# Kernel optimization log

Hardware: AMD Instinct MI355X
Metric: run time of the kernel (lower is better)

## Reference

```python
import jax, jax.numpy as jnp
import numpy as np

HID = 3584; NH = 16; NKV = 8; HD = 256; S = 3072; WIN = 2048
SOFTCAP = 50.0; QSCALE = 256.0 ** -0.5  # query_pre_attn_scalar = 256
NEG = -2.3819763e38


def _rope(x, cos, sin):
    # x: (B, S, heads, HD); cos/sin: (S, HD//2). Gemma half-split complex RoPE.
    x1, x2 = jnp.split(x, 2, axis=-1)
    c = cos[None, :, None, :]
    s = sin[None, :, None, :]
    return jnp.concatenate([x1 * c - x2 * s, x1 * s + x2 * c], axis=-1)


def setup_inputs() -> dict:
    key = jax.random.key(0)
    k1, k2, k3 = jax.random.split(key, 3)
    hidden_states = jax.random.normal(k1, (1, S, HID), jnp.float32)
    qkv_w = jax.random.normal(k2, (NH * HD + 2 * NKV * HD, HID), jnp.float32) * 0.02
    o_w = jax.random.normal(k3, (HID, NH * HD), jnp.float32) * 0.02
    inv = 1.0 / (10000.0 ** (jnp.arange(0, HD, 2, dtype=jnp.float32) / HD))
    ang = jnp.arange(S, dtype=jnp.float32)[:, None] * inv[None, :]
    freqs_cis = jnp.stack([jnp.cos(ang), jnp.sin(ang)], axis=-1)  # (S, HD//2, 2)
    kv_write_indices = jnp.arange(S, dtype=jnp.int32)
    k_cache = jnp.zeros((1, S, NKV, HD), jnp.float32)
    v_cache = jnp.zeros((1, S, NKV, HD), jnp.float32)
    i = jnp.arange(S)[:, None]
    j = jnp.arange(S)[None, :]
    mask = jnp.where(j <= i, 0.0, NEG).astype(jnp.float32)[None, None]  # causal (1,1,S,S)
    return dict(hidden_states=hidden_states, freqs_cis=freqs_cis,
                kv_write_indices=kv_write_indices, k_cache=k_cache, v_cache=v_cache,
                mask=mask, qkv_w=qkv_w, o_w=o_w)


def reference(hidden_states, freqs_cis, kv_write_indices, k_cache, v_cache, mask, qkv_w, o_w):
    B, L, _ = hidden_states.shape
    qkv = hidden_states @ qkv_w.T  # (B, L, 8192)
    xq, xk, xv = jnp.split(qkv, [NH * HD, NH * HD + NKV * HD], axis=-1)
    xq = xq.reshape(B, L, NH, HD)
    xk = xk.reshape(B, L, NKV, HD)
    xv = xv.reshape(B, L, NKV, HD)
    cos, sin = freqs_cis[..., 0], freqs_cis[..., 1]
    xq = _rope(xq, cos, sin)
    xk = _rope(xk, cos, sin)
    # KV cache index_copy_ on dim 1
    k_all = k_cache.at[:, kv_write_indices].set(xk)  # (B, T, NKV, HD)
    v_all = v_cache.at[:, kv_write_indices].set(xv)
    T = k_all.shape[1]
    G = NH // NKV  # queries per kv head; grouped einsum avoids repeat_interleave
    q = (xq * QSCALE).transpose(0, 2, 1, 3).reshape(B, NKV, G, L, HD)
    k = k_all.transpose(0, 2, 1, 3)  # (B, NKV, T, HD)
    v = v_all.transpose(0, 2, 1, 3)
    scores = jnp.einsum('bkgsd,bktd->bkgst', q, k)
    # logit softcapping
    scores = jnp.tanh(scores / SOFTCAP) * SOFTCAP
    # sliding-window band applied on top of the provided (causal) mask
    i = jnp.arange(L)[:, None]
    j = jnp.arange(T)[None, :]
    band = (j >= i - WIN + 1) & (j <= i + WIN - 1)
    m = jnp.where(band, mask, NEG)  # (1,1,L,T)
    scores = scores + m[:, :, None]  # broadcast over group dim
    probs = jax.nn.softmax(scores.astype(jnp.float32), axis=-1).astype(q.dtype)
    out = jnp.einsum('bkgst,bktd->bkgsd', probs, v)
    out = out.reshape(B, NH, L, HD).transpose(0, 2, 1, 3).reshape(B, L, NH * HD)
    return out @ o_w.T
```

## Files before the change

kernel.cpp:

```cpp
#include <hip/hip_runtime.h>

#define S_LEN 3072
#define NHQ 16
#define NKVH 8
#define HDIM 256
#define WIN 2048
#define QKV_COLS 8192

typedef __bf16 bf16x8 __attribute__((ext_vector_type(8)));
typedef float f32x4 __attribute__((ext_vector_type(4)));

__device__ __forceinline__ unsigned short f2bf(float f) {
    union { float f; unsigned u; } v; v.f = f;
    unsigned r = v.u + 0x7FFFu + ((v.u >> 16) & 1u);
    return (unsigned short)(r >> 16);
}
__device__ __forceinline__ float bf2f(unsigned short u) {
    union { unsigned u; float f; } v; v.u = ((unsigned)u) << 16; return v.f;
}

typedef __attribute__((address_space(3))) void lds_void_t;
typedef const __attribute__((address_space(1))) void glb_void_t;
__device__ __forceinline__ void async16(const void* g, void* l) {
    __builtin_amdgcn_global_load_lds((glb_void_t*)g, (lds_void_t*)l, 16, 0, 0);
}

__global__ __launch_bounds__(256) void cast_bf16_kernel(const float* __restrict__ src,
                                                        unsigned short* __restrict__ dst,
                                                        int n) {
    int i = (blockIdx.x * 256 + threadIdx.x) * 4;
    if (i >= n) return;
    float4 v = *(const float4*)(src + i);
    ushort4 o;
    o.x = f2bf(v.x); o.y = f2bf(v.y); o.z = f2bf(v.z); o.w = f2bf(v.w);
    *(ushort4*)(dst + i) = o;
}

template <int OUT_BF16>
__global__ __launch_bounds__(256) void gemm_bt(const unsigned short* __restrict__ A,
                                               const unsigned short* __restrict__ B,
                                               void* __restrict__ Cv,
                                               int N, int K) {
    __shared__ __align__(16) unsigned short At[128 * 32];
    __shared__ __align__(16) unsigned short Bt[128 * 32];
    const int tid = threadIdx.x;
    const int wid = tid >> 6, lane = tid & 63;
    const int ln = lane & 15, quad = lane >> 4;
    const int bm = blockIdx.y, bn = blockIdx.x;
    const int wm = wid >> 1, wn = wid & 1;

    const f32x4 fzero = {0.f, 0.f, 0.f, 0.f};
    f32x4 acc[4][4];
#pragma unroll
    for (int i = 0; i < 4; i++) {
#pragma unroll
        for (int j = 0; j < 4; j++) acc[i][j] = fzero;
    }

    const unsigned short* gA = A + (size_t)(bm * 128 + wid * 32 + (lane >> 2)) * K + (lane & 3) * 8;
    const unsigned short* gB = B + (size_t)(bn * 128 + wid * 32 + (lane >> 2)) * K + (lane & 3) * 8;
    unsigned short* lA = At + wid * 32 * 32;
    unsigned short* lB = Bt + wid * 32 * 32;

    for (int k0 = 0; k0 < K; k0 += 32) {
        async16(gA + k0, lA);
        async16(gA + k0 + 16 * K, lA + 16 * 32);
        async16(gB + k0, lB);
        async16(gB + k0 + 16 * K, lB + 16 * 32);
        __syncthreads();

        bf16x8 af[4], bfr[4];
#pragma unroll
        for (int mt = 0; mt < 4; mt++)
            af[mt] = *(const bf16x8*)(At + (wm * 64 + mt * 16 + ln) * 32 + quad * 8);
#pragma unroll
        for (int nt = 0; nt < 4; nt++)
            bfr[nt] = *(const bf16x8*)(Bt + (wn * 64 + nt * 16 + ln) * 32 + quad * 8);
#pragma unroll
        for (int mt = 0; mt < 4; mt++) {
#pragma unroll
            for (int nt = 0; nt < 4; nt++)
                acc[mt][nt] = __builtin_amdgcn_mfma_f32_16x16x32_bf16(af[mt], bfr[nt], acc[mt][nt], 0, 0, 0);
        }
        __syncthreads();
    }

    const int row0 = bm * 128 + wm * 64 + quad * 4;
    const int col0 = bn * 128 + wn * 64 + ln;
    if (OUT_BF16) {
        unsigned short* C = (unsigned short*)Cv;
#pragma unroll
        for (int mt = 0; mt < 4; mt++) {
#pragma unroll
            for (int nt = 0; nt < 4; nt++) {
#pragma unroll
                for (int rr = 0; rr < 4; rr++)
                    C[(size_t)(row0 + mt * 16 + rr) * N + col0 + nt * 16] = f2bf(acc[mt][nt][rr]);
            }
        }
    } else {
        float* C = (float*)Cv;
#pragma unroll
        for (int mt = 0; mt < 4; mt++) {
#pragma unroll
            for (int nt = 0; nt < 4; nt++) {
#pragma unroll
                for (int rr = 0; rr < 4; rr++)
                    C[(size_t)(row0 + mt * 16 + rr) * N + col0 + nt * 16] = acc[mt][nt][rr];
            }
        }
    }
}

__global__ __launch_bounds__(256) void rope_kernel(const unsigned short* __restrict__ qkv,
                                                   const float* __restrict__ freqs,
                                                   const int* __restrict__ kvidx,
                                                   unsigned short* __restrict__ Qb,
                                                   unsigned short* __restrict__ Kb) {
    int t = blockIdx.x * 256 + threadIdx.x;
    int d = t & 127;
    int t2 = t >> 7;
    int hh = t2 % 24;
    int pos = t2 / 24;
    if (pos >= S_LEN) return;
    float2 cs = *(const float2*)(freqs + ((size_t)pos * 128 + d) * 2);
    if (hh < NHQ) {
        const unsigned short* src = qkv + (size_t)pos * QKV_COLS + hh * HDIM + d;
        float x1 = bf2f(src[0]), x2 = bf2f(src[128]);
        float o1 = (x1 * cs.x - x2 * cs.y) * 0.0625f;
        float o2 = (x1 * cs.y + x2 * cs.x) * 0.0625f;
        unsigned short* dst = Qb + ((size_t)hh * S_LEN + pos) * HDIM + d;
        dst[0] = f2bf(o1);
        dst[128] = f2bf(o2);
    } else {
        int kvh = hh - NHQ;
        const unsigned short* src = qkv + (size_t)pos * QKV_COLS + NHQ * HDIM + kvh * HDIM + d;
        float x1 = bf2f(src[0]), x2 = bf2f(src[128]);
        float o1 = x1 * cs.x - x2 * cs.y;
        float o2 = x1 * cs.y + x2 * cs.x;
        int wpos = kvidx[pos];
        unsigned short* dst = Kb + ((size_t)kvh * S_LEN + wpos) * HDIM + d;
        dst[0] = f2bf(o1);
        dst[128] = f2bf(o2);
    }
}

__global__ __launch_bounds__(256) void vtrans_kernel(const unsigned short* __restrict__ qkv,
                                                     const int* __restrict__ kvidx,
                                                     unsigned short* __restrict__ Vbt) {
    __shared__ unsigned short T[64][72];
    int pos0 = blockIdx.x * 64;
    int c0 = blockIdx.y * 64;
    int a = threadIdx.x >> 6;
    int b = threadIdx.x & 63;
#pragma unroll
    for (int r = 0; r < 16; r++) {
        int pl = r * 4 + a;
        T[pl][b] = qkv[(size_t)(pos0 + pl) * QKV_COLS + 6144 + c0 + b];
    }
    __syncthreads();
    int wpos = kvidx[pos0 + b];
#pragma unroll
    for (int r = 0; r < 16; r++) {
        int cl = r * 4 + a;
        Vbt[(size_t)(c0 + cl) * S_LEN + wpos] = T[b][cl];
    }
}

__global__ __launch_bounds__(512, 4) void attn_kernel(const unsigned short* __restrict__ Qb,
                                                      const unsigned short* __restrict__ Kb,
                                                      const unsigned short* __restrict__ Vbt,
                                                      float* __restrict__ Acc,
                                                      float* __restrict__ Ps,
                                                      unsigned short* __restrict__ attn_out) {
    __shared__ __align__(16) unsigned short Kl[2][32 * 256];
    __shared__ __align__(16) unsigned short Vl[2][256 * 32];
    __shared__ __align__(16) unsigned short Plb[8][16][40];

    const int kv = blockIdx.x / 96;
    const int it = 95 - (blockIdx.x % 96);
    int qb, sub, nc;
    if (it < 16)      { qb = it; sub = 0; nc = 1; }
    else if (it < 48) { int e = it - 16; qb = 16 + (e >> 1); sub = e & 1; nc = 2; }
    else              { int e = it - 48; qb = 32 + e / 3; sub = e % 3; nc = 3; }

    const int q0 = qb * 64;
    const int tid = threadIdx.x;
    const int wid = tid >> 6, lane = tid & 63;
    const int ln = lane & 15, quad = lane >> 4;
    const int h = kv * 2 + (wid >> 2);
    const int wrow = (wid & 3) * 16;

    bf16x8 qf[8];
    {
        const unsigned short* qrow = Qb + ((size_t)h * S_LEN + q0 + wrow + ln) * HDIM;
#pragma unroll
        for (int k0 = 0; k0 < 8; k0++)
            qf[k0] = *(const bf16x8*)(qrow + k0 * 32 + quad * 8);
    }

    const f32x4 fzero = {0.f, 0.f, 0.f, 0.f};
    f32x4 acc[16];
#pragma unroll
    for (int t = 0; t < 16; t++) acc[t] = fzero;
    float ps[4] = {0.f, 0.f, 0.f, 0.f};

    const int imin = q0 + wrow;
    const int imax = imin + 15;
    const int irow = imin + quad * 4;

    const int t_lo = (q0 >= WIN) ? ((q0 - (WIN - 1)) >> 5) : 0;
    const int t_hi = (q0 + 63) >> 5;
    const int tn = t_hi - t_lo + 1;
    const int ts = t_lo + (tn * sub) / nc;
    const int te = t_lo + (tn * (sub + 1)) / nc;

    const unsigned short* kSrcA = Kb + ((size_t)kv * S_LEN + (tid >> 5)) * HDIM
                                  + ((tid & 31) ^ ((tid >> 5) & 7)) * 8;
    const unsigned short* vSrcA = Vbt + ((size_t)kv * HDIM + (tid >> 2)) * S_LEN
                                  + ((tid & 3) ^ ((tid >> 3) & 3)) * 8;

    {
        const int p0s = ts * 32;
        const unsigned short* ks = kSrcA + (size_t)p0s * HDIM;
        const unsigned short* vs = vSrcA + p0s;
        async16(ks,                 &Kl[0][tid * 8]);
        async16(ks + 16 * HDIM,     &Kl[0][(512 + tid) * 8]);
        async16(vs,                 &Vl[0][tid * 8]);
        async16(vs + 128 * S_LEN,   &Vl[0][(512 + tid) * 8]);
    }

    const int kswz = (ln & 7);
    const unsigned short* vbb_off = (const unsigned short*)0; (void)vbb_off;
    int cur = 0;

    for (int tt = ts; tt < te; tt++) {
        asm volatile("s_waitcnt vmcnt(0)" ::: "memory");
        __builtin_amdgcn_s_barrier();
        asm volatile("" ::: "memory");

        if (tt + 1 < te) {
            const int p0n = (tt + 1) * 32;
            const unsigned short* ks = kSrcA + (size_t)p0n * HDIM;
            const unsigned short* vs = vSrcA + p0n;
            async16(ks,                 &Kl[cur ^ 1][tid * 8]);
            async16(ks + 16 * HDIM,     &Kl[cur ^ 1][(512 + tid) * 8]);
            async16(vs,                 &Vl[cur ^ 1][tid * 8]);
            async16(vs + 128 * S_LEN,   &Vl[cur ^ 1][(512 + tid) * 8]);
        }

        const int p0 = tt * 32;
        const bool live = (p0 <= imax) && (p0 + 31 >= imin - WIN + 1);
        if (live) {
            const unsigned short* kb = Kl[cur];
            f32x4 s0 = fzero, s1 = fzero;
#pragma unroll
            for (int k0 = 0; k0 < 8; k0++) {
                const int cp = (((k0 * 4 + quad) ^ kswz) << 3);
                bf16x8 b0 = *(const bf16x8*)(kb + ln * HDIM + cp);
                s0 = __builtin_amdgcn_mfma_f32_16x16x32_bf16(qf[k0], b0, s0, 0, 0, 0);
            }
#pragma unroll
            for (int k0 = 0; k0 < 8; k0++) {
                const int cp = (((k0 * 4 + quad) ^ kswz) << 3);
                bf16x8 b1 = *(const bf16x8*)(kb + (16 + ln) * HDIM + cp);
                s1 = __builtin_amdgcn_mfma_f32_16x16x32_bf16(qf[k0], b1, s1, 0, 0, 0);
            }

            const bool full = (p0 + 31 <= imin) && (p0 >= imax - WIN + 1);
#pragma unroll
            for (int r = 0; r < 4; r++) {
                float z0 = __expf(s0[r] * 0.04f);
                float z1 = __expf(s1[r] * 0.04f);
                float t0 = fmaf(-100.f, __builtin_amdgcn_rcpf(z0 + 1.f), 50.f);
                float t1 = fmaf(-100.f, __builtin_amdgcn_rcpf(z1 + 1.f), 50.f);
                float p0v = __expf(t0);
                float p1v = __expf(t1);
                if (!full) {
                    const int i = irow + r;
                    int j0 = p0 + ln, j1 = p0 + 16 + ln;
                    p0v = ((j0 <= i) && (j0 + WIN > i)) ? p0v : 0.f;
                    p1v = ((j1 <= i) && (j1 + WIN > i)) ? p1v : 0.f;
                }
                ps[r] += p0v + p1v;
                Plb[wid][quad * 4 + r][ln] = f2bf(p0v);
                Plb[wid][quad * 4 + r][16 + ln] = f2bf(p1v);
            }
            bf16x8 pa = *(const bf16x8*)(&Plb[wid][ln][quad * 8]);
            const unsigned short* vbb = Vl[cur] + ln * 32 + ((quad ^ ((ln >> 1) & 3)) << 3);
#pragma unroll
            for (int t = 0; t < 16; t++) {
                bf16x8 vb = *(const bf16x8*)(vbb + t * 512);
                acc[t] = __builtin_amdgcn_mfma_f32_16x16x32_bf16(pa, vb, acc[t], 0, 0, 0);
            }
        }
        cur ^= 1;
    }

    float psr[4];
#pragma unroll
    for (int r = 0; r < 4; r++) {
        float s = ps[r];
#pragma unroll
        for (int o = 1; o <= 8; o <<= 1)
            s += __shfl_xor(s, o);
        psr[r] = s;
    }

    if (nc == 1) {
#pragma unroll
        for (int t = 0; t < 16; t++) {
#pragma unroll
            for (int r = 0; r < 4; r++) {
                float o = acc[t][r] * __builtin_amdgcn_rcpf(psr[r]);
                attn_out[(size_t)(irow + r) * 4096 + h * HDIM + t * 16 + ln] = f2bf(o);
            }
        }
    } else {
        if (ln == 0) {
#pragma unroll
            for (int r = 0; r < 4; r++)
                atomicAdd(&Ps[h * S_LEN + irow + r], psr[r]);
        }
#pragma unroll
        for (int t = 0; t < 16; t++) {
#pragma unroll
            for (int r = 0; r < 4; r++)
                atomicAdd(&Acc[((size_t)h * S_LEN + irow + r) * HDIM + t * 16 + ln], acc[t][r]);
        }
    }
}

__global__ __launch_bounds__(256) void norm_kernel(const float* __restrict__ Acc,
                                                   const float* __restrict__ Ps,
                                                   unsigned short* __restrict__ attn_out) {
    int row = blockIdx.x * 4 + (threadIdx.x >> 6);
    int lane = threadIdx.x & 63;
    int h = row >> 11;
    int pos = 1024 + (row & 2047);
    float4 a = *(const float4*)(Acc + ((size_t)h * S_LEN + pos) * HDIM + lane * 4);
    float inv = __builtin_amdgcn_rcpf(Ps[h * S_LEN + pos]);
    ushort4 o;
    o.x = f2bf(a.x * inv); o.y = f2bf(a.y * inv);
    o.z = f2bf(a.z * inv); o.w = f2bf(a.w * inv);
    *(ushort4*)(attn_out + (size_t)pos * 4096 + h * HDIM + lane * 4) = o;
}

extern "C" void kernel_launch(void* const* d_in, const int* in_sizes, int n_in,
                              void* d_out, int out_size, void* d_ws, size_t ws_size,
                              hipStream_t stream) {
    (void)in_sizes; (void)n_in; (void)out_size; (void)ws_size;
    const float* hidden = (const float*)d_in[0];
    const float* freqs  = (const float*)d_in[1];
    const int* kvidx    = (const int*)d_in[2];
    const float* qkv_w  = (const float*)d_in[6];
    const float* o_w    = (const float*)d_in[7];
    float* out = (float*)d_out;

    char* ws = (char*)d_ws;
    unsigned short* hs_bf   = (unsigned short*)(ws);
    unsigned short* w1_bf   = (unsigned short*)(ws + 22020096);
    unsigned short* w2_bf   = (unsigned short*)(ws + 80740352);
    unsigned short* qkv_bf  = (unsigned short*)(ws + 110100480);
    unsigned short* Qb      = (unsigned short*)(ws + 160432128);
    unsigned short* Kb      = (unsigned short*)(ws + 185597952);
    unsigned short* Vbt     = (unsigned short*)(ws + 198180864);
    unsigned short* attn_bf = (unsigned short*)(ws + 210763776);

    float* Acc = (float*)(ws + 110100480);
    float* Ps  = (float*)(ws);

    cast_bf16_kernel<<<10752, 256, 0, stream>>>(hidden, hs_bf, 11010048);
    cast_bf16_kernel<<<28672, 256, 0, stream>>>(qkv_w, w1_bf, 29360128);
    cast_bf16_kernel<<<14336, 256, 0, stream>>>(o_w, w2_bf, 14680064);

    gemm_bt<1><<<dim3(64, 24), 256, 0, stream>>>(hs_bf, w1_bf, (void*)qkv_bf, 8192, 3584);

    rope_kernel<<<36864, 256, 0, stream>>>(qkv_bf, freqs, kvidx, Qb, Kb);
    vtrans_kernel<<<dim3(48, 32), 256, 0, stream>>>(qkv_bf, kvidx, Vbt);

    hipMemsetAsync(Acc, 0, (size_t)16 * 3072 * 256 * 4, stream);
    hipMemsetAsync(Ps, 0, (size_t)16 * 3072 * 4, stream);

    attn_kernel<<<768, 512, 0, stream>>>(Qb, Kb, Vbt, Acc, Ps, attn_bf);
    norm_kernel<<<8192, 256, 0, stream>>>(Acc, Ps, attn_bf);

    gemm_bt<0><<<dim3(28, 24), 256, 0, stream>>>(attn_bf, w2_bf, (void*)out, 3584, 4096);
}
```

Baseline: 943.2 us.

## Rework attention to 32x32 MFMA tiles with per-head 128-row blocks and split-K rebalancing

The attention kernel now uses 32x32x16 bf16 MFMA instead of 16x16x32. Each 256-thread block handles one query head and 128 query rows, with each wave owning 32 rows. The KV range is split into up to five chunks to balance work, and the normalization kernel is adjusted to the new split boundaries. The GEMM also remaps workgroup ids across 8 groups, aiming for better L2 or XCD locality. Each block now loads its own KV tiles, which doubles KV traffic relative to the previous sharing across two query heads. More chunks also mean more atomic accumulation, and the larger accumulators raise register pressure.

```diff
diff --git a/kernel.cpp b/kernel.cpp
--- a/kernel.cpp
+++ b/kernel.cpp
@@ -9,6 +9,7 @@
 
 typedef __bf16 bf16x8 __attribute__((ext_vector_type(8)));
 typedef float f32x4 __attribute__((ext_vector_type(4)));
+typedef float f32x16 __attribute__((ext_vector_type(16)));
 
 __device__ __forceinline__ unsigned short f2bf(float f) {
     union { float f; unsigned u; } v; v.f = f;
@@ -46,7 +47,19 @@
     const int tid = threadIdx.x;
     const int wid = tid >> 6, lane = tid & 63;
     const int ln = lane & 15, quad = lane >> 4;
-    const int bm = blockIdx.y, bn = blockIdx.x;
+
+    int bm, bn;
+    {
+        const int nwg = gridDim.x * gridDim.y;
+        int orig = blockIdx.y * gridDim.x + blockIdx.x;
+        int wg = orig;
+        if ((nwg & 7) == 0) {
+            const int cpx = nwg >> 3;
+            wg = (orig & 7) * cpx + (orig >> 3);
+        }
+        bm = wg / gridDim.x;
+        bn = wg % gridDim.x;
+    }
     const int wm = wid >> 1, wn = wid & 1;
 
     const f32x4 fzero = {0.f, 0.f, 0.f, 0.f};
@@ -167,7 +180,7 @@
     }
 }
 
-__global__ __launch_bounds__(512, 4) void attn_kernel(const unsigned short* __restrict__ Qb,
+__global__ __launch_bounds__(256, 1) void attn_kernel(const unsigned short* __restrict__ Qb,
                                                       const unsigned short* __restrict__ Kb,
                                                       const unsigned short* __restrict__ Vbt,
                                                       float* __restrict__ Acc,
@@ -175,42 +188,47 @@
                                                       unsigned short* __restrict__ attn_out) {
     __shared__ __align__(16) unsigned short Kl[2][32 * 256];
     __shared__ __align__(16) unsigned short Vl[2][256 * 32];
-    __shared__ __align__(16) unsigned short Plb[8][16][40];
-
-    const int kv = blockIdx.x / 96;
-    const int it = 95 - (blockIdx.x % 96);
+    __shared__ __align__(16) unsigned short Plb[4][1024];
+
+    const int h = blockIdx.x / 80;
+    const int it = 79 - (blockIdx.x % 80);
     int qb, sub, nc;
-    if (it < 16)      { qb = it; sub = 0; nc = 1; }
-    else if (it < 48) { int e = it - 16; qb = 16 + (e >> 1); sub = e & 1; nc = 2; }
-    else              { int e = it - 48; qb = 32 + e / 3; sub = e % 3; nc = 3; }
-
-    const int q0 = qb * 64;
+    if (it < 4)       { qb = it; sub = 0; nc = 1; }
+    else if (it < 12) { int e = it - 4;  qb = 4 + (e >> 1); sub = e & 1;  nc = 2; }
+    else if (it < 24) { int e = it - 12; qb = 8 + e / 3;    sub = e % 3;  nc = 3; }
+    else if (it < 40) { int e = it - 24; qb = 12 + (e >> 2); sub = e & 3; nc = 4; }
+    else              { int e = it - 40; qb = 16 + e / 5;   sub = e % 5;  nc = 5; }
+
+    const int kv = h >> 1;
+    const int q0 = qb * 128;
     const int tid = threadIdx.x;
     const int wid = tid >> 6, lane = tid & 63;
-    const int ln = lane & 15, quad = lane >> 4;
-    const int h = kv * 2 + (wid >> 2);
-    const int wrow = (wid & 3) * 16;
-
-    bf16x8 qf[8];
+    const int ln32 = lane & 31, hi = lane >> 5;
+    const int qw0 = q0 + wid * 32;
+
+    bf16x8 qf[16];
     {
-        const unsigned short* qrow = Qb + ((size_t)h * S_LEN + q0 + wrow + ln) * HDIM;
-#pragma unroll
-        for (int k0 = 0; k0 < 8; k0++)
-            qf[k0] = *(const bf16x8*)(qrow + k0 * 32 + quad * 8);
-    }
-
-    const f32x4 fzero = {0.f, 0.f, 0.f, 0.f};
-    f32x4 acc[16];
-#pragma unroll
-    for (int t = 0; t < 16; t++) acc[t] = fzero;
-    float ps[4] = {0.f, 0.f, 0.f, 0.f};
-
-    const int imin = q0 + wrow;
-    const int imax = imin + 15;
-    const int irow = imin + quad * 4;
+        const unsigned short* qrow = Qb + ((size_t)h * S_LEN + qw0 + ln32) * HDIM + hi * 8;
+#pragma unroll
+        for (int s = 0; s < 16; s++)
+            qf[s] = *(const bf16x8*)(qrow + s * 16);
+    }
+
+    f32x16 pacc[8];
+#pragma unroll
+    for (int dt = 0; dt < 8; dt++) {
+#pragma unroll
+        for (int i = 0; i < 16; i++) pacc[dt][i] = 0.f;
+    }
+    float ps[16];
+#pragma unroll
+    for (int r = 0; r < 16; r++) ps[r] = 0.f;
+
+    const int imin = qw0;
+    const int imax = qw0 + 31;
 
     const int t_lo = (q0 >= WIN) ? ((q0 - (WIN - 1)) >> 5) : 0;
-    const int t_hi = (q0 + 63) >> 5;
+    const int t_hi = (q0 + 127) >> 5;
     const int tn = t_hi - t_lo + 1;
     const int ts = t_lo + (tn * sub) / nc;
     const int te = t_lo + (tn * (sub + 1)) / nc;
@@ -222,16 +240,18 @@
 
     {
         const int p0s = ts * 32;
-        const unsigned short* ks = kSrcA + (size_t)p0s * HDIM;
-        const unsigned short* vs = vSrcA + p0s;
-        async16(ks,                 &Kl[0][tid * 8]);
-        async16(ks + 16 * HDIM,     &Kl[0][(512 + tid) * 8]);
-        async16(vs,                 &Vl[0][tid * 8]);
-        async16(vs + 128 * S_LEN,   &Vl[0][(512 + tid) * 8]);
-    }
-
-    const int kswz = (ln & 7);
-    const unsigned short* vbb_off = (const unsigned short*)0; (void)vbb_off;
+        const unsigned short* ksg = kSrcA + (size_t)p0s * HDIM;
+        const unsigned short* vsg = vSrcA + p0s;
+#pragma unroll
+        for (int c = 0; c < 4; c++)
+            async16(ksg + (size_t)(c * 8) * HDIM, &Kl[0][(c * 256 + tid) * 8]);
+#pragma unroll
+        for (int c = 0; c < 4; c++)
+            async16(vsg + (size_t)(c * 64) * S_LEN, &Vl[0][(c * 256 + tid) * 8]);
+    }
+
+    unsigned short* plw = &Plb[wid][0];
+    const int kswz = ln32 & 7;
     int cur = 0;
 
     for (int tt = ts; tt < te; tt++) {
@@ -241,92 +261,95 @@
 
         if (tt + 1 < te) {
             const int p0n = (tt + 1) * 32;
-            const unsigned short* ks = kSrcA + (size_t)p0n * HDIM;
-            const unsigned short* vs = vSrcA + p0n;
-            async16(ks,                 &Kl[cur ^ 1][tid * 8]);
-            async16(ks + 16 * HDIM,     &Kl[cur ^ 1][(512 + tid) * 8]);
-            async16(vs,                 &Vl[cur ^ 1][tid * 8]);
-            async16(vs + 128 * S_LEN,   &Vl[cur ^ 1][(512 + tid) * 8]);
+            const unsigned short* ksg = kSrcA + (size_t)p0n * HDIM;
+            const unsigned short* vsg = vSrcA + p0n;
+#pragma unroll
+            for (int c = 0; c < 4; c++)
+                async16(ksg + (size_t)(c * 8) * HDIM, &Kl[cur ^ 1][(c * 256 + tid) * 8]);
+#pragma unroll
+            for (int c = 0; c < 4; c++)
+                async16(vsg + (size_t)(c * 64) * S_LEN, &Vl[cur ^ 1][(c * 256 + tid) * 8]);
         }
 
         const int p0 = tt * 32;
         const bool live = (p0 <= imax) && (p0 + 31 >= imin - WIN + 1);
         if (live) {
             const unsigned short* kb = Kl[cur];
-            f32x4 s0 = fzero, s1 = fzero;
-#pragma unroll
-            for (int k0 = 0; k0 < 8; k0++) {
-                const int cp = (((k0 * 4 + quad) ^ kswz) << 3);
-                bf16x8 b0 = *(const bf16x8*)(kb + ln * HDIM + cp);
-                s0 = __builtin_amdgcn_mfma_f32_16x16x32_bf16(qf[k0], b0, s0, 0, 0, 0);
-            }
-#pragma unroll
-            for (int k0 = 0; k0 < 8; k0++) {
-                const int cp = (((k0 * 4 + quad) ^ kswz) << 3);
-                bf16x8 b1 = *(const bf16x8*)(kb + (16 + ln) * HDIM + cp);
-                s1 = __builtin_amdgcn_mfma_f32_16x16x32_bf16(qf[k0], b1, s1, 0, 0, 0);
+            f32x16 sacc;
+#pragma unroll
+            for (int i = 0; i < 16; i++) sacc[i] = 0.f;
+#pragma unroll
+            for (int s = 0; s < 16; s++) {
+                bf16x8 kf = *(const bf16x8*)(kb + ln32 * 256 + ((((s << 1) + hi) ^ kswz) << 3));
+                sacc = __builtin_amdgcn_mfma_f32_32x32x16_bf16(qf[s], kf, sacc, 0, 0, 0);
             }
 
             const bool full = (p0 + 31 <= imin) && (p0 >= imax - WIN + 1);
 #pragma unroll
-            for (int r = 0; r < 4; r++) {
-                float z0 = __expf(s0[r] * 0.04f);
-                float z1 = __expf(s1[r] * 0.04f);
-                float t0 = fmaf(-100.f, __builtin_amdgcn_rcpf(z0 + 1.f), 50.f);
-                float t1 = fmaf(-100.f, __builtin_amdgcn_rcpf(z1 + 1.f), 50.f);
-                float p0v = __expf(t0);
-                float p1v = __expf(t1);
+            for (int r = 0; r < 16; r++) {
+                float z = __expf(sacc[r] * 0.04f);
+                float t = fmaf(-100.f, __builtin_amdgcn_rcpf(z + 1.f), 50.f);
+                float p = __expf(t);
+                const int qloc = (r & 3) + 8 * (r >> 2) + 4 * hi;
                 if (!full) {
-                    const int i = irow + r;
-                    int j0 = p0 + ln, j1 = p0 + 16 + ln;
-                    p0v = ((j0 <= i) && (j0 + WIN > i)) ? p0v : 0.f;
-                    p1v = ((j1 <= i) && (j1 + WIN > i)) ? p1v : 0.f;
+                    const int i = qw0 + qloc;
+                    const int j = p0 + ln32;
+                    p = ((j <= i) && (j + WIN > i)) ? p : 0.f;
                 }
-                ps[r] += p0v + p1v;
-                Plb[wid][quad * 4 + r][ln] = f2bf(p0v);
-                Plb[wid][quad * 4 + r][16 + ln] = f2bf(p1v);
-            }
-            bf16x8 pa = *(const bf16x8*)(&Plb[wid][ln][quad * 8]);
-            const unsigned short* vbb = Vl[cur] + ln * 32 + ((quad ^ ((ln >> 1) & 3)) << 3);
-#pragma unroll
-            for (int t = 0; t < 16; t++) {
-                bf16x8 vb = *(const bf16x8*)(vbb + t * 512);
-                acc[t] = __builtin_amdgcn_mfma_f32_16x16x32_bf16(pa, vb, acc[t], 0, 0, 0);
+                ps[r] += p;
+                plw[qloc * 32 + (((ln32 >> 3) ^ ((qloc >> 1) & 3)) << 3) + (ln32 & 7)] = f2bf(p);
+            }
+
+            bf16x8 pa0 = *(const bf16x8*)(plw + ln32 * 32 + ((hi ^ ((ln32 >> 1) & 3)) << 3));
+            bf16x8 pa1 = *(const bf16x8*)(plw + ln32 * 32 + (((2 + hi) ^ ((ln32 >> 1) & 3)) << 3));
+            const unsigned short* vb = Vl[cur];
+#pragma unroll
+            for (int dt = 0; dt < 8; dt++) {
+                const int d = dt * 32 + ln32;
+                const int vswz = (d >> 1) & 3;
+                bf16x8 v0 = *(const bf16x8*)(vb + d * 32 + ((hi ^ vswz) << 3));
+                pacc[dt] = __builtin_amdgcn_mfma_f32_32x32x16_bf16(pa0, v0, pacc[dt], 0, 0, 0);
+                bf16x8 v1 = *(const bf16x8*)(vb + d * 32 + (((2 + hi) ^ vswz) << 3));
+                pacc[dt] = __builtin_amdgcn_mfma_f32_32x32x16_bf16(pa1, v1, pacc[dt], 0, 0, 0);
             }
         }
         cur ^= 1;
     }
 
-    float psr[4];
-#pragma unroll
-    for (int r = 0; r < 4; r++) {
+#pragma unroll
+    for (int r = 0; r < 16; r++) {
         float s = ps[r];
 #pragma unroll
-        for (int o = 1; o <= 8; o <<= 1)
+        for (int o = 1; o <= 16; o <<= 1)
             s += __shfl_xor(s, o);
-        psr[r] = s;
+        ps[r] = s;
     }
 
     if (nc == 1) {
 #pragma unroll
-        for (int t = 0; t < 16; t++) {
-#pragma unroll
-            for (int r = 0; r < 4; r++) {
-                float o = acc[t][r] * __builtin_amdgcn_rcpf(psr[r]);
-                attn_out[(size_t)(irow + r) * 4096 + h * HDIM + t * 16 + ln] = f2bf(o);
+        for (int dt = 0; dt < 8; dt++) {
+#pragma unroll
+            for (int r = 0; r < 16; r++) {
+                const int q = qw0 + (r & 3) + 8 * (r >> 2) + 4 * hi;
+                float o = pacc[dt][r] * __builtin_amdgcn_rcpf(ps[r]);
+                attn_out[(size_t)q * 4096 + h * HDIM + dt * 32 + ln32] = f2bf(o);
             }
         }
     } else {
-        if (ln == 0) {
-#pragma unroll
-            for (int r = 0; r < 4; r++)
-                atomicAdd(&Ps[h * S_LEN + irow + r], psr[r]);
-        }
-#pragma unroll
-        for (int t = 0; t < 16; t++) {
-#pragma unroll
-            for (int r = 0; r < 4; r++)
-                atomicAdd(&Acc[((size_t)h * S_LEN + irow + r) * HDIM + t * 16 + ln], acc[t][r]);
+        if (ln32 == 0) {
+#pragma unroll
+            for (int r = 0; r < 16; r++) {
+                const int q = qw0 + (r & 3) + 8 * (r >> 2) + 4 * hi;
+                atomicAdd(&Ps[h * S_LEN + q], ps[r]);
+            }
+        }
+#pragma unroll
+        for (int dt = 0; dt < 8; dt++) {
+#pragma unroll
+            for (int r = 0; r < 16; r++) {
+                const int q = qw0 + (r & 3) + 8 * (r >> 2) + 4 * hi;
+                atomicAdd(&Acc[((size_t)h * S_LEN + q) * HDIM + dt * 32 + ln32], pacc[dt][r]);
+            }
         }
     }
 }
@@ -336,8 +359,8 @@
                                                    unsigned short* __restrict__ attn_out) {
     int row = blockIdx.x * 4 + (threadIdx.x >> 6);
     int lane = threadIdx.x & 63;
-    int h = row >> 11;
-    int pos = 1024 + (row & 2047);
+    int h = row / 2560;
+    int pos = 512 + (row - h * 2560);
     float4 a = *(const float4*)(Acc + ((size_t)h * S_LEN + pos) * HDIM + lane * 4);
     float inv = __builtin_amdgcn_rcpf(Ps[h * S_LEN + pos]);
     ushort4 o;
@@ -382,8 +405,8 @@
     hipMemsetAsync(Acc, 0, (size_t)16 * 3072 * 256 * 4, stream);
     hipMemsetAsync(Ps, 0, (size_t)16 * 3072 * 4, stream);
 
-    attn_kernel<<<768, 512, 0, stream>>>(Qb, Kb, Vbt, Acc, Ps, attn_bf);
-    norm_kernel<<<8192, 256, 0, stream>>>(Acc, Ps, attn_bf);
+    attn_kernel<<<1280, 256, 0, stream>>>(Qb, Kb, Vbt, Acc, Ps, attn_bf);
+    norm_kernel<<<10240, 256, 0, stream>>>(Acc, Ps, attn_bf);
 
     gemm_bt<0><<<dim3(28, 24), 256, 0, stream>>>(attn_bf, w2_bf, (void*)out, 3584, 4096);
 }
```

Measured after the change: 1.014 ms. 7.5% more time.
